# Kernel tuning notes

Hardware: AMD Instinct MI355X
Metric: run time of the kernel (lower is better)

The kernel has to match this reference:

```python
import jax, jax.numpy as jnp
import numpy as np
import math

LOG2PI = math.log(2 * math.pi)
K = 16           # num_comp
C = 64           # channels
S, NN, T = 2, 207, 12
NFEAT = S * NN * T  # 4968 = in_features of the Conv1d(k=1) projections


def setup_inputs() -> dict:
    key = jax.random.key(0)
    ks = jax.random.split(key, 7)
    x = jax.random.normal(ks[0], (8, C, S, NN, T), dtype=jnp.float32)
    scale = 0.02
    alpha_w = jax.random.normal(ks[1], (K, NFEAT), dtype=jnp.float32) * scale
    alpha_b = jax.random.normal(ks[2], (K,), dtype=jnp.float32) * scale
    sigma_w = jax.random.normal(ks[3], (K, NFEAT), dtype=jnp.float32) * scale
    sigma_b = jax.random.normal(ks[4], (K,), dtype=jnp.float32) * scale
    mu_w = jax.random.normal(ks[5], (K, NFEAT), dtype=jnp.float32) * scale
    mu_b = jax.random.normal(ks[6], (K,), dtype=jnp.float32) * scale
    return {"x": x, "alpha_w": alpha_w, "alpha_b": alpha_b,
            "sigma_w": sigma_w, "sigma_b": sigma_b, "mu_w": mu_w, "mu_b": mu_b}


def reference(x, alpha_w, alpha_b, sigma_w, sigma_b, mu_w, mu_b):
    b, c, s, n, t = x.shape
    hd = x.reshape(b, c, -1)                       # (b, c, N); torch's hd after final permute
    # Conv1d(kernel=1) over the (b, N, c) layout == per-(b,c) linear N -> K
    def proj(w, bias):
        return jnp.einsum('bcn,kn->bck', hd, w) + bias  # (b, c, K)
    alphas = jax.nn.softmax(proj(alpha_w, alpha_b), axis=-1)   # softmax over K
    sigma = jnp.exp(proj(sigma_w, sigma_b))                    # (b, c, K)
    mu = proj(mu_w, mu_b)                                      # (b, c, K)

    # log N(h | mu_k, sigma_k^2): (b, c, N, K) via broadcasting (original repeats)
    z = (hd[..., None] - mu[:, :, None, :]) / sigma[:, :, None, :]
    log_component_prob = -jnp.log(sigma)[:, :, None, :] - 0.5 * LOG2PI - 0.5 * z * z
    log_prob = log_component_prob + jnp.log(alphas)[:, :, None, :]
    # original computes log(sum(exp(.))) without max-subtraction; replicate exactly
    log_sum = jnp.log(jnp.sum(jnp.exp(log_prob), axis=-1, keepdims=True))
    weightedlogPdf = log_prob - log_sum                        # (b, c, N, K)
    labels = jnp.argmax(weightedlogPdf, axis=-1)               # (b, c, N) int

    # cluster_norm: due to torch aliasing (new_mu = new_sigma = labels, same storage),
    # both end up equal to sigma gathered by label, so norm uses sigma_g for center+scale.
    sigma_g = jnp.take_along_axis(sigma, labels, axis=2)       # (b, c, N)
    norm = (hd - sigma_g) / (sigma_g + 1e-5)
    out = norm.reshape(b, c, s, n, t)

    # probability regularization loss
    first_item = jnp.mean(jnp.exp(weightedlogPdf) * log_component_prob)
    q_z = jnp.mean(weightedlogPdf, axis=2)                     # (b, c, K)
    kl = jnp.mean(alphas * (jnp.log(alphas) - q_z))            # F.kl_div(q_z, alphas, 'mean')
    loss = kl - first_item
    return out, loss
```

## Files before the change

kernel.cpp:

```cpp
#include <hip/hip_runtime.h>
#include <math.h>

#define NROWS 512
#define NFEAT 4968
#define NVEC4 1242
#define KSLICES 6
#define SLICE4 207
#define GSL 1242
#define NGBLK (NROWS * 4)
#define WPB 20
#define NWORDS (NGBLK * WPB)
#define HALF_LOG2PI 0.91893853320467274178032973640562

__global__ __launch_bounds__(256) void proj_kernel(
    const float* __restrict__ x,
    const float* __restrict__ aw,
    const float* __restrict__ sw,
    const float* __restrict__ mw,
    double* __restrict__ pp)
{
    const int rt = blockIdx.x & 127;
    const int jg = (blockIdx.x >> 7) % 3;
    const int sl = blockIdx.x / 384;
    const int t = threadIdx.x;
    const int j = t >> 4;
    const int s16 = t & 15;
    const int row0 = rt * 4;

    const float* W = (jg == 0) ? aw : (jg == 1) ? sw : mw;
    const float4* wp = (const float4*)(W + (size_t)j * NFEAT) + sl * SLICE4;
    const float4* xp = (const float4*)(x + (size_t)row0 * NFEAT) + sl * SLICE4;

    double acc[4][2];
    #pragma unroll
    for (int r = 0; r < 4; ++r) { acc[r][0] = 0.0; acc[r][1] = 0.0; }

    for (int i = s16; i < SLICE4; i += 16) {
        float4 wv = wp[i];
        #pragma unroll
        for (int r = 0; r < 4; ++r) {
            float4 xv = xp[(size_t)r * NVEC4 + i];
            acc[r][0] = fma((double)xv.x, (double)wv.x, acc[r][0]);
            acc[r][0] = fma((double)xv.y, (double)wv.y, acc[r][0]);
            acc[r][1] = fma((double)xv.z, (double)wv.z, acc[r][1]);
            acc[r][1] = fma((double)xv.w, (double)wv.w, acc[r][1]);
        }
    }

    #pragma unroll
    for (int r = 0; r < 4; ++r) {
        double a = acc[r][0] + acc[r][1];
        #pragma unroll
        for (int off = 8; off; off >>= 1) a += __shfl_xor(a, off, 16);
        if (s16 == 0)
            pp[((size_t)(row0 + r) * 48 + jg * 16 + j) * KSLICES + sl] = a;
    }
}

__global__ __launch_bounds__(256) void params_kernel(
    const double* __restrict__ pp,
    const float* __restrict__ ab,
    const float* __restrict__ sb,
    const float* __restrict__ mb,
    double* __restrict__ mu, double* __restrict__ isg, double* __restrict__ cl,
    double* __restrict__ sig, double* __restrict__ ivp, double* __restrict__ lsg_o,
    float* __restrict__ muf, float* __restrict__ nhisg2f, float* __restrict__ clf,
    float* __restrict__ la, float* __restrict__ al)
{
    const int g = blockIdx.x * 256 + threadIdx.x;
    const int row = g >> 4, k = g & 15;
    const double* p = pp + ((size_t)row * 48 + k) * KSLICES;

    double pa = 0.0, ps = 0.0, pm = 0.0;
    #pragma unroll
    for (int s = 0; s < KSLICES; ++s) {
        pa += p[s];
        ps += p[16 * KSLICES + s];
        pm += p[32 * KSLICES + s];
    }
    pa += (double)ab[k]; ps += (double)sb[k]; pm += (double)mb[k];

    double m = pa;
    #pragma unroll
    for (int off = 8; off; off >>= 1) m = fmax(m, __shfl_xor(m, off, 16));
    double e = exp(pa - m);
    double ss = e;
    #pragma unroll
    for (int off = 8; off; off >>= 1) ss += __shfl_xor(ss, off, 16);
    double alpha = e / ss;
    double lav = log(alpha);

    double sg  = exp(ps);
    double lsg = log(sg);

    double isgv = 1.0 / sg;
    double clv  = lav - lsg - HALF_LOG2PI;

    mu[g]  = pm;
    isg[g] = isgv;
    cl[g]  = clv;
    sig[g] = sg;
    ivp[g] = 1.0 / (sg + 1e-5);
    lsg_o[g] = lsg;
    muf[g]     = (float)pm;
    nhisg2f[g] = (float)(-0.5 * isgv * isgv);
    clf[g]     = (float)clv;
    la[g]  = (float)lav;
    al[g]  = (float)alpha;
}

__global__ __launch_bounds__(256, 2) void gmm_kernel(
    const float* __restrict__ x,
    const float* __restrict__ muf, const float* __restrict__ nhisg2f,
    const float* __restrict__ clf, const float* __restrict__ laf,
    const double* __restrict__ sig, const double* __restrict__ ivp,
    float* __restrict__ out,
    double* __restrict__ shp, double* __restrict__ sh2p,
    float* __restrict__ S2p, float* __restrict__ FIp,
    unsigned long long* __restrict__ flagwords)
{
    const int row = blockIdx.x >> 2;
    const int sl  = blockIdx.x & 3;
    const int tid = threadIdx.x;
    const int g0  = row * 16;

    __shared__ double sig_s[16], ivp_s[16];
    __shared__ double redd[4][2];
    __shared__ float  redf[4][2];

    if (tid < 16) {
        sig_s[tid] = sig[g0 + tid];
        ivp_s[tid] = ivp[g0 + tid];
    }
    __syncthreads();

    float mu_r[16], ns_r[16], cl_r[16], la_r[16];
    #pragma unroll
    for (int k = 0; k < 16; ++k) {
        mu_r[k] = muf[g0 + k];
        ns_r[k] = nhisg2f[g0 + k];
        cl_r[k] = clf[g0 + k];
        la_r[k] = laf[g0 + k];
    }
    #pragma unroll
    for (int k = 0; k < 16; ++k) {
        asm volatile("" : "+v"(mu_r[k]), "+v"(ns_r[k]),
                          "+v"(cl_r[k]), "+v"(la_r[k]));
    }

    double sh = 0.0, sh2 = 0.0;
    float S2 = 0.f, FI = 0.f;

    const int base = sl * GSL;
    const float* xr = x + (size_t)row * NFEAT + base;
    float* outr = out + (size_t)row * NFEAT + base;
    const int wave = tid >> 6;
    unsigned long long* fw = flagwords + (size_t)blockIdx.x * WPB;

    for (int it = 0, n = tid; n < GSL; ++it, n += 256) {
        float h = xr[n];
        float max1 = -3.4e38f, max2 = -3.4e38f;
        int lab = 0;
        float sumexp = 0.f, s1 = 0.f;
        #pragma unroll
        for (int k = 0; k < 16; ++k) {
            float d  = h - mu_r[k];
            float lp = fmaf(d * d, ns_r[k], cl_r[k]);
            max2 = fmaxf(fminf(lp, max1), max2);
            lab  = (lp > max1) ? k : lab;
            max1 = fmaxf(lp, max1);
            float e = __expf(lp);
            sumexp += e;
            s1 = fmaf(e, lp - la_r[k], s1);
        }
        S2 += __logf(sumexp);
        FI += s1 / sumexp;
        sh += (double)h;
        sh2 = fma((double)h, (double)h, sh2);

        double sg = sig_s[lab];
        outr[n] = (float)(((double)h - sg) * ivp_s[lab]);

        unsigned long long mask = __ballot(max1 - max2 < 1e-3f);
        if ((tid & 63) == 0) fw[it * 4 + wave] = mask;
    }

    #pragma unroll
    for (int off = 32; off; off >>= 1) {
        sh  += __shfl_xor(sh,  off, 64);
        sh2 += __shfl_xor(sh2, off, 64);
        S2  += __shfl_xor(S2,  off, 64);
        FI  += __shfl_xor(FI,  off, 64);
    }
    const int lane = tid & 63;
    if (lane == 0) {
        redd[wave][0] = sh;  redd[wave][1] = sh2;
        redf[wave][0] = S2;  redf[wave][1] = FI;
    }
    __syncthreads();
    if (tid == 0) {
        shp[blockIdx.x]  = redd[0][0] + redd[1][0] + redd[2][0] + redd[3][0];
        sh2p[blockIdx.x] = redd[0][1] + redd[1][1] + redd[2][1] + redd[3][1];
        S2p[blockIdx.x]  = redf[0][0] + redf[1][0] + redf[2][0] + redf[3][0];
        FIp[blockIdx.x]  = redf[0][1] + redf[1][1] + redf[2][1] + redf[3][1];
    }
}

__global__ __launch_bounds__(256) void fixup_kernel(
    const float* __restrict__ x,
    const double* __restrict__ mu, const double* __restrict__ isg,
    const double* __restrict__ cl,
    const double* __restrict__ sig, const double* __restrict__ ivp,
    const unsigned long long* __restrict__ flagwords,
    float* __restrict__ out)
{
    for (int w = blockIdx.x * 256 + threadIdx.x; w < NWORDS; w += 128 * 256) {
        unsigned long long bits = flagwords[w];
        if (!bits) continue;
        const int blk  = w / WPB;
        const int r20  = w - blk * WPB;
        const int it   = r20 >> 2;
        const int wave = r20 & 3;
        const int row  = blk >> 2;
        const int sl   = blk & 3;
        const int g0   = row * 16;
        const int nbase = it * 256 + wave * 64;
        while (bits) {
            int b = __builtin_ctzll(bits);
            bits &= bits - 1;
            int n = nbase + b;
            if (n >= GSL) continue;
            size_t eid = (size_t)row * NFEAT + sl * GSL + n;
            double hd = (double)x[eid];
            double maxlp = -1.0e300;
            int lab = 0;
            #pragma unroll
            for (int k = 0; k < 16; ++k) {
                double zd  = (hd - mu[g0 + k]) * isg[g0 + k];
                double lpd = fma(zd * zd, -0.5, cl[g0 + k]);
                if (lpd > maxlp) { maxlp = lpd; lab = k; }
            }
            out[eid] = (float)((hd - sig[g0 + lab]) * ivp[g0 + lab]);
        }
    }
}

__global__ __launch_bounds__(1024) void loss_kernel(
    const double* __restrict__ shp, const double* __restrict__ sh2p,
    const float* __restrict__ S2p, const float* __restrict__ FIp,
    const double* __restrict__ mu, const double* __restrict__ isg,
    const double* __restrict__ lsg, const float* __restrict__ al,
    float* __restrict__ loss_out)
{
    const int tid = threadIdx.x;
    const double Nd = (double)NFEAT;

    double kl_acc = 0.0;
    for (int g = tid; g < 8192; g += 1024) {
        int row = g >> 4;
        int b = row * 4;
        double sh  = shp[b + 0] + shp[b + 1] + shp[b + 2] + shp[b + 3];
        double sh2 = sh2p[b + 0] + sh2p[b + 1] + sh2p[b + 2] + sh2p[b + 3];
        float  s2f = S2p[b + 0] + S2p[b + 1] + S2p[b + 2] + S2p[b + 3];
        double m  = mu[g];
        double iv = isg[g];
        double ns = -0.5 * iv * iv;
        double S1 = Nd * (-lsg[g] - HALF_LOG2PI)
                  + ns * (sh2 - 2.0 * m * sh + Nd * m * m);
        kl_acc += (double)al[g] * ((double)s2f - S1) / Nd;
    }
    float fi_acc = 0.f;
    for (int i = tid; i < 2048; i += 1024) fi_acc += FIp[i];

    #pragma unroll
    for (int off = 32; off; off >>= 1) {
        kl_acc += __shfl_xor(kl_acc, off, 64);
        fi_acc += __shfl_xor(fi_acc, off, 64);
    }
    __shared__ double ra[16];
    __shared__ float  rb[16];
    const int wave = tid >> 6, lane = tid & 63;
    if (lane == 0) { ra[wave] = kl_acc; rb[wave] = fi_acc; }
    __syncthreads();
    if (tid == 0) {
        double ka = 0.0; float kb = 0.f;
        #pragma unroll
        for (int i = 0; i < 16; ++i) { ka += ra[i]; kb += rb[i]; }
        loss_out[0] = (float)(ka / 8192.0 - (double)kb / 40697856.0);
    }
}

extern "C" void kernel_launch(void* const* d_in, const int* in_sizes, int n_in,
                              void* d_out, int out_size, void* d_ws, size_t ws_size,
                              hipStream_t stream) {
    const float* x  = (const float*)d_in[0];
    const float* aw = (const float*)d_in[1];
    const float* ab = (const float*)d_in[2];
    const float* sw = (const float*)d_in[3];
    const float* sb = (const float*)d_in[4];
    const float* mw = (const float*)d_in[5];
    const float* mb = (const float*)d_in[6];
    float* out = (float*)d_out;

    double* pp   = (double*)d_ws;
    double* mu   = pp + (size_t)NROWS * 48 * KSLICES;
    double* isg  = mu + 8192;
    double* cl   = isg + 8192;
    double* sig  = cl + 8192;
    double* ivp  = sig + 8192;
    double* lsg  = ivp + 8192;
    double* shp  = lsg + 8192;
    double* sh2p = shp + NGBLK;
    unsigned long long* flagwords = (unsigned long long*)(sh2p + NGBLK);
    float* muf     = (float*)(flagwords + NWORDS);
    float* nhisg2f = muf + 8192;
    float* clf     = nhisg2f + 8192;
    float* la      = clf + 8192;
    float* al      = la + 8192;
    float* S2p     = al + 8192;
    float* FIp     = S2p + NGBLK;

    proj_kernel<<<128 * 3 * KSLICES, 256, 0, stream>>>(x, aw, sw, mw, pp);
    params_kernel<<<32, 256, 0, stream>>>(pp, ab, sb, mb,
                                          mu, isg, cl, sig, ivp, lsg,
                                          muf, nhisg2f, clf, la, al);
    gmm_kernel<<<NGBLK, 256, 0, stream>>>(x, muf, nhisg2f, clf, la, sig, ivp,
                                          out, shp, sh2p, S2p, FIp, flagwords);
    fixup_kernel<<<128, 256, 0, stream>>>(x, mu, isg, cl, sig, ivp,
                                          flagwords, out);
    loss_kernel<<<1, 1024, 0, stream>>>(shp, sh2p, S2p, FIp,
                                        mu, isg, lsg, al,
                                        out + (size_t)NROWS * NFEAT);
}
```

Before: 70.38 us.

## Merge fixup and loss kernels, widen projection row tiles, use fp32 normalization

```diff
diff --git a/kernel.cpp b/kernel.cpp
--- a/kernel.cpp
+++ b/kernel.cpp
@@ -19,26 +19,26 @@
     const float* __restrict__ mw,
     double* __restrict__ pp)
 {
-    const int rt = blockIdx.x & 127;
-    const int jg = (blockIdx.x >> 7) % 3;
-    const int sl = blockIdx.x / 384;
+    const int rt = blockIdx.x & 63;
+    const int jg = (blockIdx.x >> 6) % 3;
+    const int sl = blockIdx.x / 192;
     const int t = threadIdx.x;
     const int j = t >> 4;
     const int s16 = t & 15;
-    const int row0 = rt * 4;
+    const int row0 = rt * 8;
 
     const float* W = (jg == 0) ? aw : (jg == 1) ? sw : mw;
     const float4* wp = (const float4*)(W + (size_t)j * NFEAT) + sl * SLICE4;
     const float4* xp = (const float4*)(x + (size_t)row0 * NFEAT) + sl * SLICE4;
 
-    double acc[4][2];
-    #pragma unroll
-    for (int r = 0; r < 4; ++r) { acc[r][0] = 0.0; acc[r][1] = 0.0; }
+    double acc[8][2];
+    #pragma unroll
+    for (int r = 0; r < 8; ++r) { acc[r][0] = 0.0; acc[r][1] = 0.0; }
 
     for (int i = s16; i < SLICE4; i += 16) {
         float4 wv = wp[i];
         #pragma unroll
-        for (int r = 0; r < 4; ++r) {
+        for (int r = 0; r < 8; ++r) {
             float4 xv = xp[(size_t)r * NVEC4 + i];
             acc[r][0] = fma((double)xv.x, (double)wv.x, acc[r][0]);
             acc[r][0] = fma((double)xv.y, (double)wv.y, acc[r][0]);
@@ -48,7 +48,7 @@
     }
 
     #pragma unroll
-    for (int r = 0; r < 4; ++r) {
+    for (int r = 0; r < 8; ++r) {
         double a = acc[r][0] + acc[r][1];
         #pragma unroll
         for (int off = 8; off; off >>= 1) a += __shfl_xor(a, off, 16);
@@ -65,7 +65,8 @@
     double* __restrict__ mu, double* __restrict__ isg, double* __restrict__ cl,
     double* __restrict__ sig, double* __restrict__ ivp, double* __restrict__ lsg_o,
     float* __restrict__ muf, float* __restrict__ nhisg2f, float* __restrict__ clf,
-    float* __restrict__ la, float* __restrict__ al)
+    float* __restrict__ la, float* __restrict__ al,
+    float* __restrict__ sigf, float* __restrict__ ivpf)
 {
     const int g = blockIdx.x * 256 + threadIdx.x;
     const int row = g >> 4, k = g & 15;
@@ -95,25 +96,28 @@
 
     double isgv = 1.0 / sg;
     double clv  = lav - lsg - HALF_LOG2PI;
+    double ivpv = 1.0 / (sg + 1e-5);
 
     mu[g]  = pm;
     isg[g] = isgv;
     cl[g]  = clv;
     sig[g] = sg;
-    ivp[g] = 1.0 / (sg + 1e-5);
+    ivp[g] = ivpv;
     lsg_o[g] = lsg;
     muf[g]     = (float)pm;
     nhisg2f[g] = (float)(-0.5 * isgv * isgv);
     clf[g]     = (float)clv;
-    la[g]  = (float)lav;
-    al[g]  = (float)alpha;
+    la[g]   = (float)lav;
+    al[g]   = (float)alpha;
+    sigf[g] = (float)sg;
+    ivpf[g] = (float)ivpv;
 }
 
 __global__ __launch_bounds__(256, 2) void gmm_kernel(
     const float* __restrict__ x,
     const float* __restrict__ muf, const float* __restrict__ nhisg2f,
     const float* __restrict__ clf, const float* __restrict__ laf,
-    const double* __restrict__ sig, const double* __restrict__ ivp,
+    const float* __restrict__ sigf, const float* __restrict__ ivpf,
     float* __restrict__ out,
     double* __restrict__ shp, double* __restrict__ sh2p,
     float* __restrict__ S2p, float* __restrict__ FIp,
@@ -124,13 +128,13 @@
     const int tid = threadIdx.x;
     const int g0  = row * 16;
 
-    __shared__ double sig_s[16], ivp_s[16];
+    __shared__ float sig_s[16], ivp_s[16];
     __shared__ double redd[4][2];
     __shared__ float  redf[4][2];
 
     if (tid < 16) {
-        sig_s[tid] = sig[g0 + tid];
-        ivp_s[tid] = ivp[g0 + tid];
+        sig_s[tid] = sigf[g0 + tid];
+        ivp_s[tid] = ivpf[g0 + tid];
     }
     __syncthreads();
 
@@ -174,12 +178,11 @@
             s1 = fmaf(e, lp - la_r[k], s1);
         }
         S2 += __logf(sumexp);
-        FI += s1 / sumexp;
+        FI += __fdividef(s1, sumexp);
         sh += (double)h;
         sh2 = fma((double)h, (double)h, sh2);
 
-        double sg = sig_s[lab];
-        outr[n] = (float)(((double)h - sg) * ivp_s[lab]);
+        outr[n] = (h - sig_s[lab]) * ivp_s[lab];
 
         unsigned long long mask = __ballot(max1 - max2 < 1e-3f);
         if ((tid & 63) == 0) fw[it * 4 + wave] = mask;
@@ -206,25 +209,30 @@
     }
 }
 
-__global__ __launch_bounds__(256) void fixup_kernel(
+__global__ __launch_bounds__(256) void tail_kernel(
     const float* __restrict__ x,
     const double* __restrict__ mu, const double* __restrict__ isg,
     const double* __restrict__ cl,
     const double* __restrict__ sig, const double* __restrict__ ivp,
+    const double* __restrict__ lsg, const float* __restrict__ al,
     const unsigned long long* __restrict__ flagwords,
-    float* __restrict__ out)
+    const double* __restrict__ shp, const double* __restrict__ sh2p,
+    const float* __restrict__ S2p, const float* __restrict__ FIp,
+    float* __restrict__ out, float* __restrict__ loss_out)
 {
-    for (int w = blockIdx.x * 256 + threadIdx.x; w < NWORDS; w += 128 * 256) {
+    const int tid = threadIdx.x;
+
+    for (int w = blockIdx.x * 256 + tid; w < NWORDS; w += 128 * 256) {
         unsigned long long bits = flagwords[w];
         if (!bits) continue;
         const int blk  = w / WPB;
         const int r20  = w - blk * WPB;
         const int it   = r20 >> 2;
-        const int wave = r20 & 3;
+        const int wv   = r20 & 3;
         const int row  = blk >> 2;
         const int sl   = blk & 3;
         const int g0   = row * 16;
-        const int nbase = it * 256 + wave * 64;
+        const int nbase = it * 256 + wv * 64;
         while (bits) {
             int b = __builtin_ctzll(bits);
             bits &= bits - 1;
@@ -243,50 +251,41 @@
             out[eid] = (float)((hd - sig[g0 + lab]) * ivp[g0 + lab]);
         }
     }
-}
-
-__global__ __launch_bounds__(1024) void loss_kernel(
-    const double* __restrict__ shp, const double* __restrict__ sh2p,
-    const float* __restrict__ S2p, const float* __restrict__ FIp,
-    const double* __restrict__ mu, const double* __restrict__ isg,
-    const double* __restrict__ lsg, const float* __restrict__ al,
-    float* __restrict__ loss_out)
-{
-    const int tid = threadIdx.x;
-    const double Nd = (double)NFEAT;
-
-    double kl_acc = 0.0;
-    for (int g = tid; g < 8192; g += 1024) {
-        int row = g >> 4;
-        int b = row * 4;
-        double sh  = shp[b + 0] + shp[b + 1] + shp[b + 2] + shp[b + 3];
-        double sh2 = sh2p[b + 0] + sh2p[b + 1] + sh2p[b + 2] + sh2p[b + 3];
-        float  s2f = S2p[b + 0] + S2p[b + 1] + S2p[b + 2] + S2p[b + 3];
-        double m  = mu[g];
-        double iv = isg[g];
-        double ns = -0.5 * iv * iv;
-        double S1 = Nd * (-lsg[g] - HALF_LOG2PI)
-                  + ns * (sh2 - 2.0 * m * sh + Nd * m * m);
-        kl_acc += (double)al[g] * ((double)s2f - S1) / Nd;
-    }
-    float fi_acc = 0.f;
-    for (int i = tid; i < 2048; i += 1024) fi_acc += FIp[i];
-
-    #pragma unroll
-    for (int off = 32; off; off >>= 1) {
-        kl_acc += __shfl_xor(kl_acc, off, 64);
-        fi_acc += __shfl_xor(fi_acc, off, 64);
-    }
-    __shared__ double ra[16];
-    __shared__ float  rb[16];
-    const int wave = tid >> 6, lane = tid & 63;
-    if (lane == 0) { ra[wave] = kl_acc; rb[wave] = fi_acc; }
-    __syncthreads();
-    if (tid == 0) {
-        double ka = 0.0; float kb = 0.f;
+
+    if (blockIdx.x == 0) {
+        const double Nd = (double)NFEAT;
+        double kl_acc = 0.0;
+        for (int g = tid; g < 8192; g += 256) {
+            int row = g >> 4;
+            int b = row * 4;
+            double sh  = shp[b + 0] + shp[b + 1] + shp[b + 2] + shp[b + 3];
+            double sh2 = sh2p[b + 0] + sh2p[b + 1] + sh2p[b + 2] + sh2p[b + 3];
+            float  s2f = S2p[b + 0] + S2p[b + 1] + S2p[b + 2] + S2p[b + 3];
+            double m  = mu[g];
+            double iv = isg[g];
+            double ns = -0.5 * iv * iv;
+            double S1 = Nd * (-lsg[g] - HALF_LOG2PI)
+                      + ns * (sh2 - 2.0 * m * sh + Nd * m * m);
+            kl_acc += (double)al[g] * ((double)s2f - S1) / Nd;
+        }
+        float fi_acc = 0.f;
+        for (int i = tid; i < 2048; i += 256) fi_acc += FIp[i];
+
         #pragma unroll
-        for (int i = 0; i < 16; ++i) { ka += ra[i]; kb += rb[i]; }
-        loss_out[0] = (float)(ka / 8192.0 - (double)kb / 40697856.0);
+        for (int off = 32; off; off >>= 1) {
+            kl_acc += __shfl_xor(kl_acc, off, 64);
+            fi_acc += __shfl_xor(fi_acc, off, 64);
+        }
+        __shared__ double ra[4];
+        __shared__ float  rb[4];
+        const int wv = tid >> 6, lane = tid & 63;
+        if (lane == 0) { ra[wv] = kl_acc; rb[wv] = fi_acc; }
+        __syncthreads();
+        if (tid == 0) {
+            double ka = ra[0] + ra[1] + ra[2] + ra[3];
+            float  kb = rb[0] + rb[1] + rb[2] + rb[3];
+            loss_out[0] = (float)(ka / 8192.0 - (double)kb / 40697856.0);
+        }
     }
 }
 
@@ -317,18 +316,18 @@
     float* clf     = nhisg2f + 8192;
     float* la      = clf + 8192;
     float* al      = la + 8192;
-    float* S2p     = al + 8192;
+    float* sigf    = al + 8192;
+    float* ivpf    = sigf + 8192;
+    float* S2p     = ivpf + 8192;
     float* FIp     = S2p + NGBLK;
 
-    proj_kernel<<<128 * 3 * KSLICES, 256, 0, stream>>>(x, aw, sw, mw, pp);
+    proj_kernel<<<64 * 3 * KSLICES, 256, 0, stream>>>(x, aw, sw, mw, pp);
     params_kernel<<<32, 256, 0, stream>>>(pp, ab, sb, mb,
                                           mu, isg, cl, sig, ivp, lsg,
-                                          muf, nhisg2f, clf, la, al);
-    gmm_kernel<<<NGBLK, 256, 0, stream>>>(x, muf, nhisg2f, clf, la, sig, ivp,
+                                          muf, nhisg2f, clf, la, al, sigf, ivpf);
+    gmm_kernel<<<NGBLK, 256, 0, stream>>>(x, muf, nhisg2f, clf, la, sigf, ivpf,
                                           out, shp, sh2p, S2p, FIp, flagwords);
-    fixup_kernel<<<128, 256, 0, stream>>>(x, mu, isg, cl, sig, ivp,
-                                          flagwords, out);
-    loss_kernel<<<1, 1024, 0, stream>>>(shp, sh2p, S2p, FIp,
-                                        mu, isg, lsg, al,
-                                        out + (size_t)NROWS * NFEAT);
-}
+    tail_kernel<<<128, 256, 0, stream>>>(x, mu, isg, cl, sig, ivp, lsg, al,
+                                         flagwords, shp, sh2p, S2p, FIp,
+                                         out, out + (size_t)NROWS * NFEAT);
+}
```

Result: no change. 70.40 us (+0.0%).
